# Optimization experiments

Hardware: AMD Instinct MI355X
Metric: run time of the kernel (lower is better)

The kernel has to match this reference:

```python
import jax, jax.numpy as jnp
import numpy as np

BBOX_POS_MAX = 1024.0
BN_EPS = 1e-5


def _bn_eval(x, g, b, rm, rv):
    # BatchNorm1d in eval mode: affine transform with running stats
    return g * (x - rm) * jax.lax.rsqrt(rv + BN_EPS) + b


def setup_inputs() -> dict:
    key = jax.random.key(0)
    ks = jax.random.split(key, 24)
    B, N, F = 32, 512, 1024
    E = 32768
    H1, H2, H3 = 512, 256, 128          # node_pred_hidden
    EH1, EH2 = 64, 64                   # edge_pred_hidden
    NC, EC = 8, 10                      # node/edge concept channels
    BC = 9                              # bbox_channels (4 bbox + 4 dir + 1 prio)
    s = 0.02
    inp = {
        'roi_features': jax.random.normal(ks[0], (B, N, F), jnp.float32),
        'batch_bboxes': jax.random.uniform(ks[1], (B, N, 4), jnp.float32) * BBOX_POS_MAX,
        'batch_directions': jax.random.uniform(ks[2], (B, N, 4), jnp.float32),
        'batch_priorities': jax.random.uniform(ks[3], (B, N), jnp.float32),
        'batch_edge_index': jax.random.randint(ks[4], (B, 2, E), 0, N, jnp.int32),
        # node_predictor params
        'np_w1': jax.random.normal(ks[5], (F, H1), jnp.float32) * s,
        'np_b1': jnp.zeros((H1,), jnp.float32),
        'bn1_g': jnp.ones((H1,), jnp.float32),
        'bn1_b': jnp.zeros((H1,), jnp.float32),
        'bn1_rm': jnp.zeros((H1,), jnp.float32),
        'bn1_rv': jnp.ones((H1,), jnp.float32),
        'np_w2': jax.random.normal(ks[6], (H1, H2), jnp.float32) * s,
        'np_b2': jnp.zeros((H2,), jnp.float32),
        'bn2_g': jnp.ones((H2,), jnp.float32),
        'bn2_b': jnp.zeros((H2,), jnp.float32),
        'bn2_rm': jnp.zeros((H2,), jnp.float32),
        'bn2_rv': jnp.ones((H2,), jnp.float32),
        'np_w3': jax.random.normal(ks[7], (H2, H3), jnp.float32) * s,
        'np_b3': jnp.zeros((H3,), jnp.float32),
        'ni_w': jax.random.normal(ks[8], (H3, NC), jnp.float32) * s,
        'ni_b': jnp.zeros((NC,), jnp.float32),
        # edge_predictor params (input dim = 2 * bbox_channels)
        'ep_w1': jax.random.normal(ks[9], (2 * BC, EH1), jnp.float32) * s,
        'ep_b1': jnp.zeros((EH1,), jnp.float32),
        'ep_w2': jax.random.normal(ks[10], (EH1, EH2), jnp.float32) * s,
        'ep_b2': jnp.zeros((EH2,), jnp.float32),
        'ei_w': jax.random.normal(ks[11], (EH2, EC), jnp.float32) * s,
        'ei_b': jnp.zeros((EC,), jnp.float32),
    }
    return inp


def reference(roi_features, batch_bboxes, batch_directions, batch_priorities,
              batch_edge_index,
              np_w1, np_b1, bn1_g, bn1_b, bn1_rm, bn1_rv,
              np_w2, np_b2, bn2_g, bn2_b, bn2_rm, bn2_rv,
              np_w3, np_b3, ni_w, ni_b,
              ep_w1, ep_b1, ep_w2, ep_b2, ei_w, ei_b):
    B, N, F = roi_features.shape
    # ---- node path: MLP (eval-mode BN, dropout = identity) + sigmoid interpreter
    x = roi_features.reshape(B * N, F)
    h = jax.nn.relu(_bn_eval(x @ np_w1 + np_b1, bn1_g, bn1_b, bn1_rm, bn1_rv))
    h = jax.nn.relu(_bn_eval(h @ np_w2 + np_b2, bn2_g, bn2_b, bn2_rm, bn2_rv))
    h = jax.nn.relu(h @ np_w3 + np_b3)
    node_concepts = jax.nn.sigmoid(h @ ni_w + ni_b).reshape(B, N, -1)
    # ---- edge path: per-batch gather of node attrs via edge_index, concat, MLP
    node_attr = jnp.concatenate(
        [batch_bboxes / BBOX_POS_MAX, batch_directions, batch_priorities[..., None]],
        axis=-1)  # [B, N, 9]
    C = node_attr.shape[-1]
    src_idx = batch_edge_index[:, 0, :, None]  # [B, E, 1]
    dst_idx = batch_edge_index[:, 1, :, None]
    src = jnp.take_along_axis(node_attr, src_idx.astype(jnp.int32), axis=1)  # [B, E, 9]
    dst = jnp.take_along_axis(node_attr, dst_idx.astype(jnp.int32), axis=1)
    edge_attr = jnp.concatenate([src, dst], axis=-1).reshape(-1, 2 * C)  # [B*E, 18]
    e = jax.nn.relu(edge_attr @ ep_w1 + ep_b1)
    e = jax.nn.relu(e @ ep_w2 + ep_b2)
    edge_concepts = jax.nn.sigmoid(e @ ei_w + ei_b)  # [B*E, EC]
    return node_concepts, edge_concepts
```

## Files before the change

### kernel.cpp

```cpp
#include <hip/hip_runtime.h>
#include <cstdint>
#include <cstddef>

#define BN_EPSF 1e-5f

constexpr int B_  = 32, N_ = 512, F_ = 1024, E_ = 32768;
constexpr int H1_ = 512, H2_ = 256, H3_ = 128, NC_ = 8, EC_ = 10;
constexpr int M_  = B_ * N_;
constexpr int NE_ = B_ * E_;

typedef short bf16x8 __attribute__((ext_vector_type(8)));
typedef float f32x4  __attribute__((ext_vector_type(4)));

__device__ __forceinline__ short f2bf(float f) {
  union { float f; unsigned u; } v; v.f = f;
  unsigned r = v.u + 0x7fffu + ((v.u >> 16) & 1u);
  return (short)(r >> 16);
}
__device__ __forceinline__ float bfbits(unsigned u) {
  union { unsigned u; float f; } v; v.u = u; return v.f;
}

__global__ __launch_bounds__(256) void k_f2bf(
    const float* __restrict__ in, ushort* __restrict__ out, int n8)
{
  int i = blockIdx.x * 256 + threadIdx.x;
  if (i >= n8) return;
  float4 a = *(const float4*)(in + (size_t)i * 8);
  float4 b = *(const float4*)(in + (size_t)i * 8 + 4);
  ushort o[8];
  o[0] = (ushort)f2bf(a.x); o[1] = (ushort)f2bf(a.y);
  o[2] = (ushort)f2bf(a.z); o[3] = (ushort)f2bf(a.w);
  o[4] = (ushort)f2bf(b.x); o[5] = (ushort)f2bf(b.y);
  o[6] = (ushort)f2bf(b.z); o[7] = (ushort)f2bf(b.w);
  *(uint4*)(out + (size_t)i * 8) = *(uint4*)o;
}

__global__ __launch_bounds__(256) void k_wt(
    const float* __restrict__ W, short* __restrict__ Wt, int K, int N)
{
  __shared__ float s[32][33];
  const int tx = threadIdx.x & 31, ty = threadIdx.x >> 5;
  const int k0 = blockIdx.y * 32, n0 = blockIdx.x * 32;
#pragma unroll
  for (int r = 0; r < 4; r++)
    s[ty * 4 + r][tx] = W[(size_t)(k0 + ty * 4 + r) * N + n0 + tx];
  __syncthreads();
#pragma unroll
  for (int r = 0; r < 4; r++)
    Wt[(size_t)(n0 + ty * 4 + r) * K + k0 + tx] = f2bf(s[tx][ty * 4 + r]);
}

template <int EPI>
__global__ __launch_bounds__(256) void k_gemm_mfma(
    const short* __restrict__ A, const short* __restrict__ Wt,
    const float* __restrict__ bias,
    const float* __restrict__ g, const float* __restrict__ bb,
    const float* __restrict__ rm, const float* __restrict__ rv,
    short* __restrict__ C, int M, int K, int N)
{
  __shared__ short As[128 * 32];
  __shared__ short Bs[128 * 32];

  const int tid  = threadIdx.x;
  const int wave = tid >> 6, lane = tid & 63;
  const int m0 = blockIdx.y * 128, n0 = blockIdx.x * 128;
  const int wm = wave >> 1, wn = wave & 1;

  const int arow = tid >> 2;
  const int akq  = (tid & 3) * 8;

  f32x4 acc[4][4] = {};

  for (int k0 = 0; k0 < K; k0 += 32) {
#pragma unroll
    for (int it = 0; it < 2; it++) {
      const short* gp = A + (size_t)(m0 + it * 64 + arow) * K + k0 + akq;
      char* lp = (char*)As + it * 4096 + wave * 1024;
      __builtin_amdgcn_global_load_lds(
          (const __attribute__((address_space(1))) void*)gp,
          (__attribute__((address_space(3))) void*)lp, 16, 0, 0);
    }
#pragma unroll
    for (int it = 0; it < 2; it++) {
      const short* gp = Wt + (size_t)(n0 + it * 64 + arow) * K + k0 + akq;
      char* lp = (char*)Bs + it * 4096 + wave * 1024;
      __builtin_amdgcn_global_load_lds(
          (const __attribute__((address_space(1))) void*)gp,
          (__attribute__((address_space(3))) void*)lp, 16, 0, 0);
    }
    __syncthreads();

    const int ko = (lane >> 4) * 8;
    bf16x8 af[4], bfr[4];
#pragma unroll
    for (int t = 0; t < 4; t++) {
      af[t]  = *(const bf16x8*)&As[(wm * 64 + t * 16 + (lane & 15)) * 32 + ko];
      bfr[t] = *(const bf16x8*)&Bs[(wn * 64 + t * 16 + (lane & 15)) * 32 + ko];
    }
#pragma unroll
    for (int ti = 0; ti < 4; ti++)
#pragma unroll
      for (int tj = 0; tj < 4; tj++)
        acc[ti][tj] = __builtin_amdgcn_mfma_f32_16x16x32_bf16(
            af[ti], bfr[tj], acc[ti][tj], 0, 0, 0);
    __syncthreads();
  }

#pragma unroll
  for (int tj = 0; tj < 4; tj++) {
    const int col = n0 + wn * 64 + tj * 16 + (lane & 15);
    const float bi = bias[col];
    float s = 1.f, t = 0.f;
    if (EPI == 0) {
      s = g[col] * rsqrtf(rv[col] + BN_EPSF);
      t = bb[col] - rm[col] * s;
    }
#pragma unroll
    for (int ti = 0; ti < 4; ti++) {
      const int rbase = m0 + wm * 64 + ti * 16 + ((lane >> 4) << 2);
#pragma unroll
      for (int r = 0; r < 4; r++) {
        float v = acc[ti][tj][r] + bi;
        if (EPI == 0) v = fmaf(v, s, t);
        v = fmaxf(v, 0.f);
        C[(size_t)(rbase + r) * N + col] = f2bf(v);
      }
    }
  }
}

__global__ __launch_bounds__(256) void k_node_attr(
    const float* __restrict__ bbox, const float* __restrict__ dir,
    const float* __restrict__ pri, float* __restrict__ na)
{
  int i = blockIdx.x * 256 + threadIdx.x;
  if (i >= M_) return;
  float4 b = *(const float4*)(bbox + (size_t)i * 4);
  float4 d = *(const float4*)(dir + (size_t)i * 4);
  float p = pri[i];
  const float inv = 1.0f / 1024.0f;
  float* o = na + (size_t)i * 12;
  *(float4*)(o + 0) = make_float4(b.x * inv, b.y * inv, b.z * inv, b.w * inv);
  *(float4*)(o + 4) = make_float4(d.x, d.y, d.z, d.w);
  *(float4*)(o + 8) = make_float4(p, 0.f, 0.f, 0.f);
}

__global__ __launch_bounds__(256) void k_node_head(
    const ushort* __restrict__ h3, const float* __restrict__ w,
    const float* __restrict__ b, float* __restrict__ out)
{
  __shared__ __align__(16) float sw[H3_ * NC_];
  __shared__ float sb[NC_];
  for (int i = threadIdx.x; i < H3_ * NC_; i += 256) sw[i] = w[i];
  if (threadIdx.x < NC_) sb[threadIdx.x] = b[threadIdx.x];
  __syncthreads();

  int row = blockIdx.x * 256 + threadIdx.x;
  if (row >= M_) return;
  const ushort* hr = h3 + (size_t)row * H3_;
  float acc[NC_];
#pragma unroll
  for (int c = 0; c < NC_; c++) acc[c] = sb[c];
  for (int k = 0; k < H3_; k += 8) {
    uint4 u = *(const uint4*)&hr[k];
    float hv[8];
    hv[0] = bfbits(u.x << 16); hv[1] = bfbits(u.x & 0xffff0000u);
    hv[2] = bfbits(u.y << 16); hv[3] = bfbits(u.y & 0xffff0000u);
    hv[4] = bfbits(u.z << 16); hv[5] = bfbits(u.z & 0xffff0000u);
    hv[6] = bfbits(u.w << 16); hv[7] = bfbits(u.w & 0xffff0000u);
#pragma unroll
    for (int kk = 0; kk < 8; kk++)
#pragma unroll
      for (int c = 0; c < NC_; c++)
        acc[c] = fmaf(hv[kk], sw[(k + kk) * NC_ + c], acc[c]);
  }
  float4 o1, o2;
  float* p1 = (float*)&o1; float* p2 = (float*)&o2;
#pragma unroll
  for (int c = 0; c < 4; c++) {
    p1[c] = 1.f / (1.f + __expf(-acc[c]));
    p2[c] = 1.f / (1.f + __expf(-acc[c + 4]));
  }
  *(float4*)&out[(size_t)row * NC_ + 0] = o1;
  *(float4*)&out[(size_t)row * NC_ + 4] = o2;
}

__global__ __launch_bounds__(256, 2) void k_edge_mfma(
    const float* __restrict__ na, const int* __restrict__ eidx,
    const float* __restrict__ w1, const float* __restrict__ b1,
    const float* __restrict__ w2, const float* __restrict__ b2,
    const float* __restrict__ wo, const float* __restrict__ bo,
    float* __restrict__ out)
{
  __shared__ __align__(16) short sA[9216];
  __shared__ __align__(16) short sH1[128 * 72];
  __shared__ float sB[144];

  const int tid  = threadIdx.x;
  const int wave = tid >> 6, lane = tid & 63;
  const int lm  = lane & 15;
  const int lk8 = (lane >> 4) * 8;
  const int lr  = (lane >> 4) * 4;

  short* sW1 = sA;
  short* sW2 = sA + 2048;
  short* sW3 = sA + 6144;
  short* sX  = sA;
  short* sH2 = sA;

  for (int i = tid; i < 2048; i += 256) {
    int n = i >> 5, k = i & 31;
    sW1[i] = (k < 18) ? f2bf(w1[k * 64 + n]) : (short)0;
  }
  for (int i = tid; i < 4096; i += 256) {
    int n = i >> 6, k = i & 63;
    sW2[i] = f2bf(w2[k * 64 + n]);
  }
  for (int i = tid; i < 1024; i += 256) {
    int n = i >> 6, k = i & 63;
    sW3[i] = (n < 10) ? f2bf(wo[k * 10 + n]) : (short)0;
  }
  if (tid < 64) { sB[tid] = b1[tid]; sB[64 + tid] = b2[tid]; }
  if (tid < 16) sB[128 + tid] = (tid < 10) ? bo[tid] : 0.f;
  __syncthreads();

  bf16x8 fW1[4], fW2[4][2], fW3[2];
#pragma unroll
  for (int t = 0; t < 4; t++)
    fW1[t] = *(const bf16x8*)&sW1[(t * 16 + lm) * 32 + lk8];
#pragma unroll
  for (int t = 0; t < 4; t++)
#pragma unroll
    for (int ks = 0; ks < 2; ks++)
      fW2[t][ks] = *(const bf16x8*)&sW2[(t * 16 + lm) * 64 + ks * 32 + lk8];
#pragma unroll
  for (int ks = 0; ks < 2; ks++)
    fW3[ks] = *(const bf16x8*)&sW3[lm * 64 + ks * 32 + lk8];
  float bias1v[4], bias2v[4];
#pragma unroll
  for (int t = 0; t < 4; t++) {
    bias1v[t] = sB[t * 16 + lm];
    bias2v[t] = sB[64 + t * 16 + lm];
  }
  const float biasOv = sB[128 + lm];
  __syncthreads();

  for (int bi = 0; bi < 8; bi++) {
    const int e0 = (blockIdx.x * 8 + bi) * 128;

    if (tid < 128) {
      int e = e0 + tid;
      int b = e >> 15, kk = e & (E_ - 1);
      const int* ei = eidx + (size_t)b * 2 * E_;
      int s = ei[kk], d = ei[E_ + kk];
      const float* ps = na + ((size_t)b * N_ + s) * 12;
      const float* pd = na + ((size_t)b * N_ + d) * 12;
      float4 a0 = *(const float4*)(ps);
      float4 a1 = *(const float4*)(ps + 4);
      float  a2 = ps[8];
      float4 c0 = *(const float4*)(pd);
      float4 c1 = *(const float4*)(pd + 4);
      float  c2 = pd[8];
      ushort xr[32];
      xr[0] = (ushort)f2bf(a0.x); xr[1] = (ushort)f2bf(a0.y);
      xr[2] = (ushort)f2bf(a0.z); xr[3] = (ushort)f2bf(a0.w);
      xr[4] = (ushort)f2bf(a1.x); xr[5] = (ushort)f2bf(a1.y);
      xr[6] = (ushort)f2bf(a1.z); xr[7] = (ushort)f2bf(a1.w);
      xr[8] = (ushort)f2bf(a2);
      xr[9]  = (ushort)f2bf(c0.x); xr[10] = (ushort)f2bf(c0.y);
      xr[11] = (ushort)f2bf(c0.z); xr[12] = (ushort)f2bf(c0.w);
      xr[13] = (ushort)f2bf(c1.x); xr[14] = (ushort)f2bf(c1.y);
      xr[15] = (ushort)f2bf(c1.z); xr[16] = (ushort)f2bf(c1.w);
      xr[17] = (ushort)f2bf(c2);
#pragma unroll
      for (int i = 18; i < 32; i++) xr[i] = 0;
      ushort* row = (ushort*)&sX[tid * 40];
      *(uint4*)(row + 0)  = *(uint4*)&xr[0];
      *(uint4*)(row + 8)  = *(uint4*)&xr[8];
      *(uint4*)(row + 16) = *(uint4*)&xr[16];
      *(uint4*)(row + 24) = *(uint4*)&xr[24];
    }
    __syncthreads();

    bf16x8 a1f[2];
#pragma unroll
    for (int ti = 0; ti < 2; ti++)
      a1f[ti] = *(const bf16x8*)&sX[(wave * 32 + ti * 16 + lm) * 40 + lk8];
    f32x4 acc1[2][4] = {};
#pragma unroll
    for (int ti = 0; ti < 2; ti++)
#pragma unroll
      for (int tj = 0; tj < 4; tj++)
        acc1[ti][tj] = __builtin_amdgcn_mfma_f32_16x16x32_bf16(
            a1f[ti], fW1[tj], acc1[ti][tj], 0, 0, 0);
#pragma unroll
    for (int ti = 0; ti < 2; ti++)
#pragma unroll
      for (int tj = 0; tj < 4; tj++)
#pragma unroll
        for (int r = 0; r < 4; r++) {
          int row = wave * 32 + ti * 16 + lr + r;
          float v = acc1[ti][tj][r] + bias1v[tj];
          sH1[row * 72 + tj * 16 + lm] = f2bf(fmaxf(v, 0.f));
        }
    __syncthreads();

    bf16x8 a2f[2][2];
#pragma unroll
    for (int ti = 0; ti < 2; ti++)
#pragma unroll
      for (int ks = 0; ks < 2; ks++)
        a2f[ti][ks] = *(const bf16x8*)&sH1[(wave * 32 + ti * 16 + lm) * 72 + ks * 32 + lk8];
    f32x4 acc2[2][4] = {};
#pragma unroll
    for (int ks = 0; ks < 2; ks++)
#pragma unroll
      for (int ti = 0; ti < 2; ti++)
#pragma unroll
        for (int tj = 0; tj < 4; tj++)
          acc2[ti][tj] = __builtin_amdgcn_mfma_f32_16x16x32_bf16(
              a2f[ti][ks], fW2[tj][ks], acc2[ti][tj], 0, 0, 0);
#pragma unroll
    for (int ti = 0; ti < 2; ti++)
#pragma unroll
      for (int tj = 0; tj < 4; tj++)
#pragma unroll
        for (int r = 0; r < 4; r++) {
          int row = wave * 32 + ti * 16 + lr + r;
          float v = acc2[ti][tj][r] + bias2v[tj];
          sH2[row * 72 + tj * 16 + lm] = f2bf(fmaxf(v, 0.f));
        }

    bf16x8 a3f[2][2];
#pragma unroll
    for (int ti = 0; ti < 2; ti++)
#pragma unroll
      for (int ks = 0; ks < 2; ks++)
        a3f[ti][ks] = *(const bf16x8*)&sH2[(wave * 32 + ti * 16 + lm) * 72 + ks * 32 + lk8];
    f32x4 acc3[2] = {};
#pragma unroll
    for (int ks = 0; ks < 2; ks++)
#pragma unroll
      for (int ti = 0; ti < 2; ti++)
        acc3[ti] = __builtin_amdgcn_mfma_f32_16x16x32_bf16(
            a3f[ti][ks], fW3[ks], acc3[ti], 0, 0, 0);
    if (lm < 10) {
#pragma unroll
      for (int ti = 0; ti < 2; ti++)
#pragma unroll
        for (int r = 0; r < 4; r++) {
          int row = wave * 32 + ti * 16 + lr + r;
          float v = acc3[ti][r] + biasOv;
          out[(size_t)(e0 + row) * 10 + lm] = 1.f / (1.f + __expf(-v));
        }
    }
    __syncthreads();
  }
}

extern "C" void kernel_launch(void* const* d_in, const int* in_sizes, int n_in,
                              void* d_out, int out_size, void* d_ws, size_t ws_size,
                              hipStream_t stream)
{
  const float* roi   = (const float*)d_in[0];
  const float* bbox  = (const float*)d_in[1];
  const float* dir   = (const float*)d_in[2];
  const float* pri   = (const float*)d_in[3];
  const int*   eidx  = (const int*)d_in[4];
  const float* w1    = (const float*)d_in[5];
  const float* b1    = (const float*)d_in[6];
  const float* g1    = (const float*)d_in[7];
  const float* bb1   = (const float*)d_in[8];
  const float* rm1   = (const float*)d_in[9];
  const float* rv1   = (const float*)d_in[10];
  const float* w2    = (const float*)d_in[11];
  const float* b2    = (const float*)d_in[12];
  const float* g2    = (const float*)d_in[13];
  const float* bb2   = (const float*)d_in[14];
  const float* rm2   = (const float*)d_in[15];
  const float* rv2   = (const float*)d_in[16];
  const float* w3    = (const float*)d_in[17];
  const float* b3    = (const float*)d_in[18];
  const float* niw   = (const float*)d_in[19];
  const float* nib   = (const float*)d_in[20];
  const float* ew1   = (const float*)d_in[21];
  const float* eb1   = (const float*)d_in[22];
  const float* ew2   = (const float*)d_in[23];
  const float* eb2   = (const float*)d_in[24];
  const float* eow   = (const float*)d_in[25];
  const float* eob   = (const float*)d_in[26];

  float* out_node = (float*)d_out;
  float* out_edge = (float*)d_out + (size_t)M_ * NC_;

  char* w = (char*)d_ws;
  short*  roiB = (short*)w;
  short*  h2   = (short*)w;
  ushort* h3   = (ushort*)(w + 8388608);
  short*  h1   = (short*)(w + 33554432);
  short*  w1t  = (short*)(w + 33554432 + 16777216);
  short*  w2t  = (short*)(w + 33554432 + 16777216 + 1048576);
  short*  w3t  = (short*)(w + 33554432 + 16777216 + 1310720);
  float*  na   = (float*)(w + 33554432 + 16777216 + 1376256);

  k_node_attr<<<M_ / 256, 256, 0, stream>>>(bbox, dir, pri, na);
  k_edge_mfma<<<NE_ / (8 * 128), 256, 0, stream>>>(
      na, eidx, ew1, eb1, ew2, eb2, eow, eob, out_edge);

  k_f2bf<<<(M_ * F_ / 8) / 256, 256, 0, stream>>>(roi, (ushort*)roiB, M_ * F_ / 8);
  k_wt<<<dim3(H1_ / 32, F_ / 32), 256, 0, stream>>>(w1, w1t, F_, H1_);
  k_wt<<<dim3(H2_ / 32, H1_ / 32), 256, 0, stream>>>(w2, w2t, H1_, H2_);
  k_wt<<<dim3(H3_ / 32, H2_ / 32), 256, 0, stream>>>(w3, w3t, H2_, H3_);

  k_gemm_mfma<0><<<dim3(H1_ / 128, M_ / 128), 256, 0, stream>>>(
      roiB, w1t, b1, g1, bb1, rm1, rv1, h1, M_, F_, H1_);
  k_gemm_mfma<0><<<dim3(H2_ / 128, M_ / 128), 256, 0, stream>>>(
      h1, w2t, b2, g2, bb2, rm2, rv2, h2, M_, H1_, H2_);
  k_gemm_mfma<1><<<dim3(H3_ / 128, M_ / 128), 256, 0, stream>>>(
      h2, w3t, b3, nullptr, nullptr, nullptr, nullptr, (short*)h3, M_, H1_ / 2, H3_);

  k_node_head<<<M_ / 256, 256, 0, stream>>>(h3, niw, nib, out_node);
}
```

Before: 285.0 us.

## Fuse node MLP into one per-row-tile kernel and merge prep kernels

Replaces the three separate node GEMM kernels and the node head with one kernel. Each block owns 32 rows and chains layer1 -> layer2 -> layer3 -> head in LDS, with the head done on MFMA, so the h1/h2/h3 intermediates no longer round-trip through global memory. The bf16 conversion, weight transposes and node-attr prep are merged into one launch, and packing now uses perm. The trade-off is that the 32-row tiles reload all of w1t per block, giving 512 blocks with lower data reuse and possibly less MFMA efficiency than the 128x128 tiles.

Result: faster. 274.5 us (-3.7%).

```diff
diff --git a/kernel.cpp b/kernel.cpp
--- a/kernel.cpp
+++ b/kernel.cpp
@@ -17,31 +17,22 @@
   unsigned r = v.u + 0x7fffu + ((v.u >> 16) & 1u);
   return (short)(r >> 16);
 }
-__device__ __forceinline__ float bfbits(unsigned u) {
-  union { unsigned u; float f; } v; v.u = u; return v.f;
-}
-
-__global__ __launch_bounds__(256) void k_f2bf(
-    const float* __restrict__ in, ushort* __restrict__ out, int n8)
+__device__ __forceinline__ unsigned rnepack(float a, float b) {
+  unsigned ua = __float_as_uint(a); ua = ua + 0x7fffu + ((ua >> 16) & 1u);
+  unsigned ub = __float_as_uint(b); ub = ub + 0x7fffu + ((ub >> 16) & 1u);
+  return __builtin_amdgcn_perm(ub, ua, 0x07060302u);
+}
+
+#define GLDS(gp, lp) __builtin_amdgcn_global_load_lds( \
+    (const __attribute__((address_space(1))) void*)(gp), \
+    (__attribute__((address_space(3))) void*)(lp), 16, 0, 0)
+
+__device__ __forceinline__ void wt_body(
+    const float* __restrict__ W, short* __restrict__ Wt, int K, int N,
+    int bx, int by, float (*s)[33])
 {
-  int i = blockIdx.x * 256 + threadIdx.x;
-  if (i >= n8) return;
-  float4 a = *(const float4*)(in + (size_t)i * 8);
-  float4 b = *(const float4*)(in + (size_t)i * 8 + 4);
-  ushort o[8];
-  o[0] = (ushort)f2bf(a.x); o[1] = (ushort)f2bf(a.y);
-  o[2] = (ushort)f2bf(a.z); o[3] = (ushort)f2bf(a.w);
-  o[4] = (ushort)f2bf(b.x); o[5] = (ushort)f2bf(b.y);
-  o[6] = (ushort)f2bf(b.z); o[7] = (ushort)f2bf(b.w);
-  *(uint4*)(out + (size_t)i * 8) = *(uint4*)o;
-}
-
-__global__ __launch_bounds__(256) void k_wt(
-    const float* __restrict__ W, short* __restrict__ Wt, int K, int N)
-{
-  __shared__ float s[32][33];
   const int tx = threadIdx.x & 31, ty = threadIdx.x >> 5;
-  const int k0 = blockIdx.y * 32, n0 = blockIdx.x * 32;
+  const int k0 = by * 32, n0 = bx * 32;
 #pragma unroll
   for (int r = 0; r < 4; r++)
     s[ty * 4 + r][tx] = W[(size_t)(k0 + ty * 4 + r) * N + n0 + tx];
@@ -51,139 +42,199 @@
     Wt[(size_t)(n0 + ty * 4 + r) * K + k0 + tx] = f2bf(s[tx][ty * 4 + r]);
 }
 
-template <int EPI>
-__global__ __launch_bounds__(256) void k_gemm_mfma(
-    const short* __restrict__ A, const short* __restrict__ Wt,
-    const float* __restrict__ bias,
-    const float* __restrict__ g, const float* __restrict__ bb,
-    const float* __restrict__ rm, const float* __restrict__ rv,
-    short* __restrict__ C, int M, int K, int N)
-{
-  __shared__ short As[128 * 32];
-  __shared__ short Bs[128 * 32];
-
-  const int tid  = threadIdx.x;
-  const int wave = tid >> 6, lane = tid & 63;
-  const int m0 = blockIdx.y * 128, n0 = blockIdx.x * 128;
-  const int wm = wave >> 1, wn = wave & 1;
-
-  const int arow = tid >> 2;
-  const int akq  = (tid & 3) * 8;
-
-  f32x4 acc[4][4] = {};
-
-  for (int k0 = 0; k0 < K; k0 += 32) {
-#pragma unroll
-    for (int it = 0; it < 2; it++) {
-      const short* gp = A + (size_t)(m0 + it * 64 + arow) * K + k0 + akq;
-      char* lp = (char*)As + it * 4096 + wave * 1024;
-      __builtin_amdgcn_global_load_lds(
-          (const __attribute__((address_space(1))) void*)gp,
-          (__attribute__((address_space(3))) void*)lp, 16, 0, 0);
-    }
-#pragma unroll
-    for (int it = 0; it < 2; it++) {
-      const short* gp = Wt + (size_t)(n0 + it * 64 + arow) * K + k0 + akq;
-      char* lp = (char*)Bs + it * 4096 + wave * 1024;
-      __builtin_amdgcn_global_load_lds(
-          (const __attribute__((address_space(1))) void*)gp,
-          (__attribute__((address_space(3))) void*)lp, 16, 0, 0);
-    }
-    __syncthreads();
-
-    const int ko = (lane >> 4) * 8;
-    bf16x8 af[4], bfr[4];
-#pragma unroll
-    for (int t = 0; t < 4; t++) {
-      af[t]  = *(const bf16x8*)&As[(wm * 64 + t * 16 + (lane & 15)) * 32 + ko];
-      bfr[t] = *(const bf16x8*)&Bs[(wn * 64 + t * 16 + (lane & 15)) * 32 + ko];
-    }
-#pragma unroll
-    for (int ti = 0; ti < 4; ti++)
-#pragma unroll
-      for (int tj = 0; tj < 4; tj++)
-        acc[ti][tj] = __builtin_amdgcn_mfma_f32_16x16x32_bf16(
-            af[ti], bfr[tj], acc[ti][tj], 0, 0, 0);
-    __syncthreads();
-  }
-
-#pragma unroll
-  for (int tj = 0; tj < 4; tj++) {
-    const int col = n0 + wn * 64 + tj * 16 + (lane & 15);
-    const float bi = bias[col];
-    float s = 1.f, t = 0.f;
-    if (EPI == 0) {
-      s = g[col] * rsqrtf(rv[col] + BN_EPSF);
-      t = bb[col] - rm[col] * s;
-    }
-#pragma unroll
-    for (int ti = 0; ti < 4; ti++) {
-      const int rbase = m0 + wm * 64 + ti * 16 + ((lane >> 4) << 2);
-#pragma unroll
-      for (int r = 0; r < 4; r++) {
-        float v = acc[ti][tj][r] + bi;
-        if (EPI == 0) v = fmaf(v, s, t);
-        v = fmaxf(v, 0.f);
-        C[(size_t)(rbase + r) * N + col] = f2bf(v);
-      }
-    }
-  }
-}
-
-__global__ __launch_bounds__(256) void k_node_attr(
+__global__ __launch_bounds__(256) void k_prep(
+    const float* __restrict__ roi, ushort* __restrict__ roiB,
+    const float* __restrict__ w1, short* __restrict__ w1t,
+    const float* __restrict__ w2, short* __restrict__ w2t,
+    const float* __restrict__ w3, short* __restrict__ w3t,
     const float* __restrict__ bbox, const float* __restrict__ dir,
     const float* __restrict__ pri, float* __restrict__ na)
 {
-  int i = blockIdx.x * 256 + threadIdx.x;
-  if (i >= M_) return;
-  float4 b = *(const float4*)(bbox + (size_t)i * 4);
-  float4 d = *(const float4*)(dir + (size_t)i * 4);
-  float p = pri[i];
-  const float inv = 1.0f / 1024.0f;
-  float* o = na + (size_t)i * 12;
-  *(float4*)(o + 0) = make_float4(b.x * inv, b.y * inv, b.z * inv, b.w * inv);
-  *(float4*)(o + 4) = make_float4(d.x, d.y, d.z, d.w);
-  *(float4*)(o + 8) = make_float4(p, 0.f, 0.f, 0.f);
-}
-
-__global__ __launch_bounds__(256) void k_node_head(
-    const ushort* __restrict__ h3, const float* __restrict__ w,
-    const float* __restrict__ b, float* __restrict__ out)
+  __shared__ float s[32][33];
+  const int bx = blockIdx.x;
+  if (bx < 8192) {
+    int i = bx * 256 + threadIdx.x;
+    float4 a = *(const float4*)(roi + (size_t)i * 8);
+    float4 b = *(const float4*)(roi + (size_t)i * 8 + 4);
+    unsigned o[4];
+    o[0] = rnepack(a.x, a.y); o[1] = rnepack(a.z, a.w);
+    o[2] = rnepack(b.x, b.y); o[3] = rnepack(b.z, b.w);
+    *(uint4*)(roiB + (size_t)i * 8) = *(uint4*)o;
+  } else if (bx < 8704) {
+    int idx = bx - 8192; wt_body(w1, w1t, F_, H1_, idx & 15, idx >> 4, s);
+  } else if (bx < 8832) {
+    int idx = bx - 8704; wt_body(w2, w2t, H1_, H2_, idx & 7, idx >> 3, s);
+  } else if (bx < 8864) {
+    int idx = bx - 8832; wt_body(w3, w3t, H2_, H3_, idx & 3, idx >> 2, s);
+  } else {
+    int i = (bx - 8864) * 256 + threadIdx.x;
+    float4 b = *(const float4*)(bbox + (size_t)i * 4);
+    float4 d = *(const float4*)(dir + (size_t)i * 4);
+    float p = pri[i];
+    const float inv = 1.0f / 1024.0f;
+    float* o = na + (size_t)i * 12;
+    *(float4*)(o + 0) = make_float4(b.x * inv, b.y * inv, b.z * inv, b.w * inv);
+    *(float4*)(o + 4) = make_float4(d.x, d.y, d.z, d.w);
+    *(float4*)(o + 8) = make_float4(p, 0.f, 0.f, 0.f);
+  }
+}
+
+__global__ __launch_bounds__(256) void k_node_fused(
+    const short* __restrict__ roiB, const short* __restrict__ w1t,
+    const short* __restrict__ w2t, const short* __restrict__ w3t,
+    const float* __restrict__ b1, const float* __restrict__ g1,
+    const float* __restrict__ bb1, const float* __restrict__ rm1,
+    const float* __restrict__ rv1,
+    const float* __restrict__ b2, const float* __restrict__ g2,
+    const float* __restrict__ bb2, const float* __restrict__ rm2,
+    const float* __restrict__ rv2,
+    const float* __restrict__ b3, const float* __restrict__ niw,
+    const float* __restrict__ nib, float* __restrict__ out)
 {
-  __shared__ __align__(16) float sw[H3_ * NC_];
-  __shared__ float sb[NC_];
-  for (int i = threadIdx.x; i < H3_ * NC_; i += 256) sw[i] = w[i];
-  if (threadIdx.x < NC_) sb[threadIdx.x] = b[threadIdx.x];
+  __shared__ short sA[2 * 32 * 32];
+  __shared__ short sStage[256 * 32];
+  __shared__ short sH1c[32 * 136];
+  __shared__ short sH2[32 * 264];
+
+  const int tid  = threadIdx.x;
+  const int wave = tid >> 6, lane = tid & 63;
+  const int lm = lane & 15, q = lane >> 4;
+  const int wm = wave >> 1, wn = wave & 1;
+  const int m0 = blockIdx.x * 32;
+
+  const int srow2 = tid >> 2;
+  const int skq2  = (tid & 3) * 8;
+
+  f32x4 acc2[8] = {};
+
+  for (int n1 = 0; n1 < 4; n1++) {
+    f32x4 acc1[4] = {};
+    for (int k0 = 0; k0 < 1024; k0 += 64) {
+      {
+        int c = tid >> 7, row = (tid >> 2) & 31;
+        GLDS(roiB + (size_t)(m0 + row) * 1024 + k0 + c * 32 + skq2,
+             (char*)sA + wave * 1024);
+      }
+#pragma unroll
+      for (int it = 0; it < 2; it++)
+#pragma unroll
+        for (int c = 0; c < 2; c++)
+          GLDS(w1t + (size_t)(n1 * 128 + it * 64 + srow2) * 1024 + k0 + c * 32 + skq2,
+               (char*)sStage + c * 8192 + it * 4096 + wave * 1024);
+      __syncthreads();
+
+      bf16x8 af[2];
+      af[0] = *(const bf16x8*)&sA[(wm * 16 + lm) * 32 + q * 8];
+      af[1] = *(const bf16x8*)&sA[1024 + (wm * 16 + lm) * 32 + q * 8];
+#pragma unroll
+      for (int nt = 0; nt < 4; nt++)
+#pragma unroll
+        for (int c = 0; c < 2; c++) {
+          bf16x8 bfr = *(const bf16x8*)&sStage[c * 4096 + (wn * 64 + nt * 16 + lm) * 32 + q * 8];
+          acc1[nt] = __builtin_amdgcn_mfma_f32_16x16x32_bf16(af[c], bfr, acc1[nt], 0, 0, 0);
+        }
+      __syncthreads();
+    }
+#pragma unroll
+    for (int nt = 0; nt < 4; nt++) {
+      int cl = wn * 64 + nt * 16 + lm;
+      int col = n1 * 128 + cl;
+      float s = g1[col] * rsqrtf(rv1[col] + BN_EPSF);
+      float t = bb1[col] - rm1[col] * s;
+      float bi = b1[col];
+#pragma unroll
+      for (int r = 0; r < 4; r++) {
+        float v = fmaf(acc1[nt][r] + bi, s, t);
+        sH1c[(wm * 16 + q * 4 + r) * 136 + cl] = f2bf(fmaxf(v, 0.f));
+      }
+    }
+    __syncthreads();
+    for (int kc = 0; kc < 4; kc++) {
+#pragma unroll
+      for (int it = 0; it < 4; it++)
+        GLDS(w2t + (size_t)(it * 64 + srow2) * 512 + n1 * 128 + kc * 32 + skq2,
+             (char*)sStage + it * 4096 + wave * 1024);
+      __syncthreads();
+      bf16x8 af2 = *(const bf16x8*)&sH1c[(wm * 16 + lm) * 136 + kc * 32 + q * 8];
+#pragma unroll
+      for (int nt = 0; nt < 8; nt++) {
+        bf16x8 bfr = *(const bf16x8*)&sStage[(wn * 128 + nt * 16 + lm) * 32 + q * 8];
+        acc2[nt] = __builtin_amdgcn_mfma_f32_16x16x32_bf16(af2, bfr, acc2[nt], 0, 0, 0);
+      }
+      __syncthreads();
+    }
+  }
+
+#pragma unroll
+  for (int nt = 0; nt < 8; nt++) {
+    int col = wn * 128 + nt * 16 + lm;
+    float s = g2[col] * rsqrtf(rv2[col] + BN_EPSF);
+    float t = bb2[col] - rm2[col] * s;
+    float bi = b2[col];
+#pragma unroll
+    for (int r = 0; r < 4; r++) {
+      float v = fmaf(acc2[nt][r] + bi, s, t);
+      sH2[(wm * 16 + q * 4 + r) * 264 + col] = f2bf(fmaxf(v, 0.f));
+    }
+  }
   __syncthreads();
 
-  int row = blockIdx.x * 256 + threadIdx.x;
-  if (row >= M_) return;
-  const ushort* hr = h3 + (size_t)row * H3_;
-  float acc[NC_];
-#pragma unroll
-  for (int c = 0; c < NC_; c++) acc[c] = sb[c];
-  for (int k = 0; k < H3_; k += 8) {
-    uint4 u = *(const uint4*)&hr[k];
-    float hv[8];
-    hv[0] = bfbits(u.x << 16); hv[1] = bfbits(u.x & 0xffff0000u);
-    hv[2] = bfbits(u.y << 16); hv[3] = bfbits(u.y & 0xffff0000u);
-    hv[4] = bfbits(u.z << 16); hv[5] = bfbits(u.z & 0xffff0000u);
-    hv[6] = bfbits(u.w << 16); hv[7] = bfbits(u.w & 0xffff0000u);
-#pragma unroll
-    for (int kk = 0; kk < 8; kk++)
-#pragma unroll
-      for (int c = 0; c < NC_; c++)
-        acc[c] = fmaf(hv[kk], sw[(k + kk) * NC_ + c], acc[c]);
-  }
-  float4 o1, o2;
-  float* p1 = (float*)&o1; float* p2 = (float*)&o2;
-#pragma unroll
-  for (int c = 0; c < 4; c++) {
-    p1[c] = 1.f / (1.f + __expf(-acc[c]));
-    p2[c] = 1.f / (1.f + __expf(-acc[c + 4]));
-  }
-  *(float4*)&out[(size_t)row * NC_ + 0] = o1;
-  *(float4*)&out[(size_t)row * NC_ + 4] = o2;
+  f32x4 acc3[4] = {};
+  for (int k0 = 0; k0 < 256; k0 += 64) {
+#pragma unroll
+    for (int it = 0; it < 2; it++)
+#pragma unroll
+      for (int c = 0; c < 2; c++)
+        GLDS(w3t + (size_t)(it * 64 + srow2) * 256 + k0 + c * 32 + skq2,
+             (char*)sStage + c * 8192 + it * 4096 + wave * 1024);
+    __syncthreads();
+#pragma unroll
+    for (int c = 0; c < 2; c++) {
+      bf16x8 af3 = *(const bf16x8*)&sH2[(wm * 16 + lm) * 264 + k0 + c * 32 + q * 8];
+#pragma unroll
+      for (int nt = 0; nt < 4; nt++) {
+        bf16x8 bfr = *(const bf16x8*)&sStage[c * 4096 + (wn * 64 + nt * 16 + lm) * 32 + q * 8];
+        acc3[nt] = __builtin_amdgcn_mfma_f32_16x16x32_bf16(af3, bfr, acc3[nt], 0, 0, 0);
+      }
+    }
+    __syncthreads();
+  }
+  short* sH3 = sH1c;
+#pragma unroll
+  for (int nt = 0; nt < 4; nt++) {
+    int col = wn * 64 + nt * 16 + lm;
+    float bi = b3[col];
+#pragma unroll
+    for (int r = 0; r < 4; r++) {
+      float v = acc3[nt][r] + bi;
+      sH3[(wm * 16 + q * 4 + r) * 136 + col] = f2bf(fmaxf(v, 0.f));
+    }
+  }
+  __syncthreads();
+
+  if (wave < 2) {
+    f32x4 a4 = {};
+#pragma unroll
+    for (int c = 0; c < 4; c++) {
+      ushort tmp[8];
+#pragma unroll
+      for (int j = 0; j < 8; j++) {
+        int k = c * 32 + q * 8 + j;
+        tmp[j] = (lm < 8) ? (ushort)f2bf(niw[k * 8 + lm]) : (ushort)0;
+      }
+      bf16x8 fw = *(bf16x8*)tmp;
+      bf16x8 af4 = *(const bf16x8*)&sH3[(wave * 16 + lm) * 136 + c * 32 + q * 8];
+      a4 = __builtin_amdgcn_mfma_f32_16x16x32_bf16(af4, fw, a4, 0, 0, 0);
+    }
+    if (lm < 8) {
+      float bi = nib[lm];
+#pragma unroll
+      for (int r = 0; r < 4; r++) {
+        float v = a4[r] + bi;
+        out[(size_t)(m0 + wave * 16 + q * 4 + r) * 8 + lm] = 1.f / (1.f + __expf(-v));
+      }
+    }
+  }
 }
 
 __global__ __launch_bounds__(256, 2) void k_edge_mfma(
@@ -396,29 +447,20 @@
 
   char* w = (char*)d_ws;
   short*  roiB = (short*)w;
-  short*  h2   = (short*)w;
-  ushort* h3   = (ushort*)(w + 8388608);
-  short*  h1   = (short*)(w + 33554432);
-  short*  w1t  = (short*)(w + 33554432 + 16777216);
-  short*  w2t  = (short*)(w + 33554432 + 16777216 + 1048576);
-  short*  w3t  = (short*)(w + 33554432 + 16777216 + 1310720);
-  float*  na   = (float*)(w + 33554432 + 16777216 + 1376256);
-
-  k_node_attr<<<M_ / 256, 256, 0, stream>>>(bbox, dir, pri, na);
-  k_edge_mfma<<<NE_ / (8 * 128), 256, 0, stream>>>(
+  short*  w1t  = (short*)(w + 33554432);
+  short*  w2t  = (short*)(w + 34603008);
+  short*  w3t  = (short*)(w + 34865152);
+  float*  na   = (float*)(w + 34930688);
+
+  k_prep<<<8928, 256, 0, stream>>>(roi, (ushort*)roiB, w1, w1t, w2, w2t,
+                                   w3, w3t, bbox, dir, pri, na);
+
+  k_edge_mfma<<<NE_ / 1024, 256, 0, stream>>>(
       na, eidx, ew1, eb1, ew2, eb2, eow, eob, out_edge);
 
-  k_f2bf<<<(M_ * F_ / 8) / 256, 256, 0, stream>>>(roi, (ushort*)roiB, M_ * F_ / 8);
-  k_wt<<<dim3(H1_ / 32, F_ / 32), 256, 0, stream>>>(w1, w1t, F_, H1_);
-  k_wt<<<dim3(H2_ / 32, H1_ / 32), 256, 0, stream>>>(w2, w2t, H1_, H2_);
-  k_wt<<<dim3(H3_ / 32, H2_ / 32), 256, 0, stream>>>(w3, w3t, H2_, H3_);
-
-  k_gemm_mfma<0><<<dim3(H1_ / 128, M_ / 128), 256, 0, stream>>>(
-      roiB, w1t, b1, g1, bb1, rm1, rv1, h1, M_, F_, H1_);
-  k_gemm_mfma<0><<<dim3(H2_ / 128, M_ / 128), 256, 0, stream>>>(
-      h1, w2t, b2, g2, bb2, rm2, rv2, h2, M_, H1_, H2_);
-  k_gemm_mfma<1><<<dim3(H3_ / 128, M_ / 128), 256, 0, stream>>>(
-      h2, w3t, b3, nullptr, nullptr, nullptr, nullptr, (short*)h3, M_, H1_ / 2, H3_);
-
-  k_node_head<<<M_ / 256, 256, 0, stream>>>(h3, niw, nib, out_node);
-}
+  k_node_fused<<<M_ / 32, 256, 0, stream>>>(
+      roiB, w1t, w2t, w3t,
+      b1, g1, bb1, rm1, rv1,
+      b2, g2, bb2, rm2, rv2,
+      b3, niw, nib, out_node);
+}
```
